# Kernel optimization log

Measured on AMD Instinct MI355X. Metric: run time of the kernel, lower is better.

## Reference

```python
import jax, jax.numpy as jnp
import numpy as np
from jax import lax

EPS = 1e-10

def _ln(x, g, b):
    m = x.mean(-1, keepdims=True)
    v = x.var(-1, keepdims=True)
    return (x - m) / jnp.sqrt(v + 1e-5) * g + b

def _gather(t, idx):
    # t: (B, HW, c), idx: (B, HW, d) -> (B, HW, d, c); out[n,i,k,:] = t[n, idx[n,i,k], :]
    return jax.vmap(lambda tn, In: tn[In])(t, idx)

def setup_inputs() -> dict:
    key = jax.random.key(0)
    ks = jax.random.split(key, 20)
    b, v, c, d, h, w, hid, ksz = 2, 2, 128, 64, 64, 64, 256, 5
    hw = h * w
    Bf = b * v  # v_1 == 1 target view per reference view
    std = 0.02
    return {
        'features_mv': jax.random.normal(ks[0], (b, v, c, h, w), jnp.float32),
        'warp_indices': jax.random.randint(ks[1], (Bf, hw, d), 0, hw, jnp.int32),
        'depth_prob': jax.random.uniform(ks[2], (Bf, hw, d), jnp.float32),
        'ln1_g': jnp.ones((c,), jnp.float32), 'ln1_b': jnp.zeros((c,), jnp.float32),
        'wq': jax.random.normal(ks[3], (c, c), jnp.float32) * std, 'bq': jnp.zeros((c,), jnp.float32),
        'wk': jax.random.normal(ks[4], (c, c), jnp.float32) * std, 'bk': jnp.zeros((c,), jnp.float32),
        'wv': jax.random.normal(ks[5], (c, c), jnp.float32) * std, 'bv': jnp.zeros((c,), jnp.float32),
        'k_pe': jax.random.normal(ks[6], (1, 1, d), jnp.float32) * std,
        'v_pe': jax.random.normal(ks[7], (1, 1, d), jnp.float32) * std,
        'rpe': jax.random.normal(ks[8], (1, 1, d), jnp.float32) * std,
        'proj_w': jax.random.normal(ks[9], (c, c), jnp.float32) * std, 'proj_b': jnp.zeros((c,), jnp.float32),
        'ln2_g': jnp.ones((c,), jnp.float32), 'ln2_b': jnp.zeros((c,), jnp.float32),
        'fc1_w': jax.random.normal(ks[10], (c, hid), jnp.float32) * std, 'fc1_b': jnp.zeros((hid,), jnp.float32),
        'dw_w': jax.random.normal(ks[11], (hid, 1, ksz, ksz), jnp.float32) * std, 'dw_b': jnp.zeros((hid,), jnp.float32),
        'fc2_w': jax.random.normal(ks[12], (hid, c), jnp.float32) * std, 'fc2_b': jnp.zeros((c,), jnp.float32),
    }

def reference(features_mv, warp_indices, depth_prob, ln1_g, ln1_b, wq, bq, wk, bk, wv, bv,
              k_pe, v_pe, rpe, proj_w, proj_b, ln2_g, ln2_b, fc1_w, fc1_b, dw_w, dw_b, fc2_w, fc2_b):
    b, v, c, h, w = features_mv.shape
    hw = h * w
    hid = fc1_w.shape[1]
    scale = c ** (-0.5)  # num_heads = 1 -> head_dim = dim

    # (b v) (h w) c
    x = features_mv.reshape(b * v, c, hw).transpose(0, 2, 1)
    shortcut = x
    xn = _ln(x, ln1_g, ln1_b)
    q = xn @ wq + bq
    k = xn @ wk + bk
    vv = xn @ wv + bv

    # nn pairing: v=2, v_1=1 -> each reference view attends the other view
    Q = (q.reshape(b, v, hw, c) * scale).reshape(b * v, hw, c)
    K = k.reshape(b, v, hw, c)[:, ::-1].reshape(b * v, hw, c)
    V = vv.reshape(b, v, hw, c)[:, ::-1].reshape(b * v, hw, c)

    # SMM_QmK: cost[n,i,k] = sum_c Q[n,i,c] * K[n, idx[n,i,k], c]
    Kg = _gather(K, warp_indices)                       # (B, hw, d, c)
    cost = jnp.einsum('bic,bikc->bik', Q, Kg)
    Q_pe = Q.sum(-1, keepdims=True)                     # (B, hw, 1)
    cost = cost + Q_pe * k_pe + rpe                     # broadcast (1,1,d)

    # (Sim_UNet similarity refinement omitted: UNetModel source unavailable; identity here)
    attn = jax.nn.softmax(cost, axis=-1)
    attn = attn * depth_prob
    attn = (attn + EPS) / (attn.sum(-1, keepdims=True) + EPS)

    # SMM_AmV: out[n,i,c] = sum_k attn[n,i,k] * V[n, idx[n,i,k], c]
    Vg = _gather(V, warp_indices)                       # (B, hw, d, c)
    out = jnp.einsum('bik,bikc->bic', attn, Vg)
    out = out + (attn * v_pe).sum(-1, keepdims=True)

    # projection + residual (v_1 == 1 so B == b*v)
    x = shortcut + (out @ proj_w + proj_b)

    # ConvFFN residual branch
    xn2 = _ln(x, ln2_g, ln2_b)
    y = jax.nn.gelu(xn2 @ fc1_w + fc1_b, approximate=False)
    yi = y.transpose(0, 2, 1).reshape(b * v, hid, h, w)
    yc = lax.conv_general_dilated(yi, dw_w, (1, 1), 'SAME', feature_group_count=hid,
                                  dimension_numbers=('NCHW', 'OIHW', 'NCHW'))
    yc = jax.nn.gelu(yc + dw_b[None, :, None, None], approximate=False)
    y = y + yc.reshape(b * v, hid, hw).transpose(0, 2, 1)
    y = y @ fc2_w + fc2_b
    return x + y
```

## Files before the change

kernel.cpp:

```cpp
#include <hip/hip_runtime.h>
#include <math.h>

#define TOK   16384
#define HW    4096
#define C     128
#define D     64
#define HID   256

constexpr float LN_EPS = 1e-5f;
constexpr float EPS_R  = 1e-10f;
constexpr float QSCALE = 0.08838834764831845f;

typedef __attribute__((ext_vector_type(8))) short  bf16x8;
typedef __attribute__((ext_vector_type(4))) float  f32x4;
typedef __attribute__((ext_vector_type(2))) _Float16 half2v;
#define MFMA16(a, b, c) __builtin_amdgcn_mfma_f32_16x16x32_bf16((a), (b), (c), 0, 0, 0)

__device__ __forceinline__ float bflo(unsigned u) { return __uint_as_float(u << 16); }
__device__ __forceinline__ float bfhi(unsigned u) { return __uint_as_float(u & 0xffff0000u); }
__device__ __forceinline__ float bfu(unsigned short u) { return __uint_as_float((unsigned)u << 16); }
__device__ __forceinline__ unsigned short f2bf(float f) {
  unsigned u = __float_as_uint(f);
  unsigned r = (u + 0x7fffu + ((u >> 16) & 1u)) >> 16;
  return (unsigned short)r;
}
__device__ __forceinline__ unsigned short f2h(float f) {
  _Float16 h = (_Float16)f;
  unsigned short r;
  __builtin_memcpy(&r, &h, 2);
  return r;
}
__device__ __forceinline__ float gelu_exact(float x) {
  return 0.5f * x * (1.0f + erff(x * 0.7071067811865476f));
}

union U4H { uint4 v; half2v h[4]; };
union U1H { unsigned v; half2v h; };

#if __has_builtin(__builtin_amdgcn_fdot2)
__device__ __forceinline__ float dot2h(half2v a, half2v b, float c) {
  return __builtin_amdgcn_fdot2(a, b, c, false);
}
#else
__device__ __forceinline__ float dot2h(half2v a, half2v b, float c) {
  return c + (float)a.x * (float)b.x + (float)a.y * (float)b.y;
}
#endif

__global__ __launch_bounds__(256) void k_prepln1(const float* __restrict__ wq,
    const float* __restrict__ wk, const float* __restrict__ wv,
    const float* __restrict__ pw, const float* __restrict__ f1w,
    const float* __restrict__ f2w, unsigned short* __restrict__ wt,
    const float* __restrict__ feat, const float* __restrict__ g,
    const float* __restrict__ b, unsigned short* __restrict__ xnb) {
  __shared__ float tile[64][C + 1];
  int bidx = blockIdx.x;
  if (bidx < 512) {
    int id = bidx * 256 + threadIdx.x;
    if (id < 16384) {
      int n = id >> 7, k = id & 127;
      wt[id] = f2bf(wq[k * 128 + n]);
    } else if (id < 32768) {
      int e = id - 16384; int n = e >> 7, k = e & 127;
      wt[id] = f2bf(wk[k * 128 + n]);
    } else if (id < 49152) {
      int e = id - 32768; int n = e >> 7, k = e & 127;
      wt[id] = f2bf(wv[k * 128 + n]);
    } else if (id < 65536) {
      int e = id - 49152; int n = e >> 7, k = e & 127;
      wt[id] = f2bf(pw[k * 128 + n]);
    } else if (id < 98304) {
      int e = id - 65536; int n = e >> 7, k = e & 127;
      wt[id] = f2bf(f1w[k * 256 + n]);
    } else {
      int e = id - 98304; int n = e >> 8, k = e & 255;
      wt[id] = f2bf(f2w[k * 128 + n]);
    }
    return;
  }
  int t0 = (bidx - 512) * 64;
  int n = t0 / HW, i0 = t0 % HW;
  int tid = threadIdx.x;
  const float* fb = feat + (size_t)n * C * HW;
  for (int e = tid; e < 64 * C; e += 256) {
    int ch = e >> 6, ii = e & 63;
    tile[ii][ch] = fb[(size_t)ch * HW + i0 + ii];
  }
  __syncthreads();
  int wave = tid >> 6, lane = tid & 63;
  for (int tkn = wave; tkn < 64; tkn += 4) {
    float a0 = tile[tkn][lane];
    float a1 = tile[tkn][lane + 64];
    float s = a0 + a1;
    for (int off = 32; off; off >>= 1) s += __shfl_xor(s, off, 64);
    float mean = s * (1.0f / 128.0f);
    float d0 = a0 - mean, d1 = a1 - mean;
    float v = d0 * d0 + d1 * d1;
    for (int off = 32; off; off >>= 1) v += __shfl_xor(v, off, 64);
    float rstd = rsqrtf(v * (1.0f / 128.0f) + LN_EPS);
    size_t ro = (size_t)(t0 + tkn) * C;
    xnb[ro + lane]      = f2bf(d0 * rstd * g[lane] + b[lane]);
    xnb[ro + lane + 64] = f2bf(d1 * rstd * g[lane + 64] + b[lane + 64]);
  }
}

__global__ __launch_bounds__(256) void k_qkv(const unsigned short* __restrict__ xnb,
    const unsigned short* __restrict__ wt,
    const float* __restrict__ bq, const float* __restrict__ bk,
    const float* __restrict__ bv, unsigned short* __restrict__ qh,
    unsigned short* __restrict__ ksw, unsigned short* __restrict__ vsw) {
  int w = threadIdx.x >> 6, lane = threadIdx.x & 63;
  int q4 = lane >> 4, m = lane & 15;
  int t0 = blockIdx.x * 64 + w * 16;
  int wsel = blockIdx.y;
  const unsigned short* Wt = wt + wsel * 16384;
  const unsigned short* ap = xnb + (size_t)(t0 + m) * C + q4 * 8;
  bf16x8 a[4];
  #pragma unroll
  for (int ks = 0; ks < 4; ks++) a[ks] = *(const bf16x8*)(ap + ks * 32);
  f32x4 acc[8];
  #pragma unroll
  for (int nt = 0; nt < 8; nt++) acc[nt] = (f32x4){0.f, 0.f, 0.f, 0.f};
  #pragma unroll
  for (int nt = 0; nt < 8; nt++) {
    const unsigned short* bp = Wt + (size_t)(nt * 16 + m) * C + q4 * 8;
    #pragma unroll
    for (int ks = 0; ks < 4; ks++) {
      bf16x8 bfrag = *(const bf16x8*)(bp + ks * 32);
      acc[nt] = MFMA16(a[ks], bfrag, acc[nt]);
    }
  }
  const float* B = (wsel == 0) ? bq : ((wsel == 1) ? bk : bv);
  float sc = (wsel == 0) ? QSCALE : 1.0f;
  unsigned short* O = (wsel == 0) ? qh : ((wsel == 1) ? ksw : vsw);
  int n = t0 >> 12, i0 = t0 & 4095;
  int base = (wsel == 0) ? t0 : (((n ^ 1) << 12) + i0);
  #pragma unroll
  for (int nt = 0; nt < 8; nt++) {
    int col = nt * 16 + m;
    float bb = B[col];
    #pragma unroll
    for (int reg = 0; reg < 4; reg++) {
      int row = base + q4 * 4 + reg;
      O[(size_t)row * C + col] = f2h((acc[nt][reg] + bb) * sc);
    }
  }
}

__global__ __launch_bounds__(256) void k_attn(const unsigned short* __restrict__ qh,
    const unsigned short* __restrict__ ksw, const unsigned short* __restrict__ vsw,
    const int* __restrict__ widx, const float* __restrict__ dprob,
    const float* __restrict__ kpe, const float* __restrict__ vpe,
    const float* __restrict__ rpe, unsigned short* __restrict__ aoutb) {
  int lane = threadIdx.x & 63;
  int wave = threadIdx.x >> 6;
  int bid = blockIdx.x;
  int n = (bid >> 1) & 3;
  int within = ((bid >> 3) << 1) | (bid & 1);
  int token = n * HW + within * 4 + wave;
  const unsigned short* Kb = ksw + (size_t)n * HW * C;
  const unsigned short* Vb = vsw + (size_t)n * HW * C;
  int g = lane >> 3, s = lane & 7;
  int myidx = widx[token * D + lane];
  float mydp = dprob[token * D + lane];
  half2v qreg[8];
  {
    const unsigned short* qp = qh + (size_t)token * C + s * 16;
    U4H qa, qb2;
    qa.v = *(const uint4*)(qp);
    qb2.v = *(const uint4*)(qp + 8);
    #pragma unroll
    for (int i = 0; i < 4; i++) { qreg[i] = qa.h[i]; qreg[4 + i] = qb2.h[i]; }
  }
  half2v ones = {(_Float16)1.0f, (_Float16)1.0f};
  float qpe = 0.f;
  #pragma unroll
  for (int i = 0; i < 8; i++) qpe = dot2h(qreg[i], ones, qpe);
  qpe += __shfl_xor(qpe, 1, 64);
  qpe += __shfl_xor(qpe, 2, 64);
  qpe += __shfl_xor(qpe, 4, 64);
  int rowv[8];
  #pragma unroll
  for (int pass = 0; pass < 8; ++pass)
    rowv[pass] = __shfl(myidx, pass * 8 + g, 64);
  uint4 ka[8], kb[8];
  #pragma unroll
  for (int pass = 0; pass < 8; ++pass) {
    const unsigned short* kr = Kb + (size_t)rowv[pass] * C + s * 16;
    ka[pass] = *(const uint4*)(kr);
    kb[pass] = *(const uint4*)(kr + 8);
  }
  float mycost = 0.f;
  #pragma unroll
  for (int pass = 0; pass < 8; ++pass) {
    U4H ua, ub;
    ua.v = ka[pass]; ub.v = kb[pass];
    float p = 0.f;
    #pragma unroll
    for (int i = 0; i < 4; i++) p = dot2h(ua.h[i], qreg[i], p);
    #pragma unroll
    for (int i = 0; i < 4; i++) p = dot2h(ub.h[i], qreg[4 + i], p);
    p += __shfl_xor(p, 1, 64);
    p += __shfl_xor(p, 2, 64);
    p += __shfl_xor(p, 4, 64);
    float t = __shfl(p, (lane & 7) << 3, 64);
    if (pass == g) mycost = t;
  }
  mycost += qpe * kpe[lane] + rpe[lane];
  float mx = mycost;
  for (int off = 32; off; off >>= 1) mx = fmaxf(mx, __shfl_xor(mx, off, 64));
  float e = __expf(mycost - mx);
  float ssum = e;
  for (int off = 32; off; off >>= 1) ssum += __shfl_xor(ssum, off, 64);
  float attn = (e / ssum) * mydp;
  float s2 = attn;
  for (int off = 32; off; off >>= 1) s2 += __shfl_xor(s2, off, 64);
  attn = (attn + EPS_R) / (s2 + EPS_R);
  float vpt = attn * vpe[lane];
  for (int off = 32; off; off >>= 1) vpt += __shfl_xor(vpt, off, 64);
  float o0 = vpt, o1 = vpt;
  unsigned att_u = __float_as_uint(attn);
  #pragma unroll
  for (int blk = 0; blk < 8; ++blk) {
    unsigned vv[8];
    #pragma unroll
    for (int j = 0; j < 8; j++) {
      int row = __builtin_amdgcn_readlane(myidx, blk * 8 + j);
      vv[j] = *(const unsigned*)(Vb + (size_t)row * C + lane * 2);
    }
    #pragma unroll
    for (int j = 0; j < 8; j++) {
      float a = __uint_as_float(__builtin_amdgcn_readlane(att_u, blk * 8 + j));
      U1H h; h.v = vv[j];
      o0 += a * (float)h.h.x;
      o1 += a * (float)h.h.y;
    }
  }
  unsigned pk = (unsigned)f2bf(o0) | ((unsigned)f2bf(o1) << 16);
  *(unsigned*)(aoutb + (size_t)token * C + lane * 2) = pk;
}

__global__ __launch_bounds__(256) void k_projln(const unsigned short* __restrict__ aoutb,
    const unsigned short* __restrict__ wt, const float* __restrict__ pb,
    const float* __restrict__ feat, float* __restrict__ xio,
    const float* __restrict__ g2, const float* __restrict__ b2,
    unsigned short* __restrict__ xn2b) {
  int w = threadIdx.x >> 6, lane = threadIdx.x & 63;
  int q4 = lane >> 4, m = lane & 15;
  int t0 = blockIdx.x * 64 + w * 16;
  const unsigned short* Wt = wt + 3 * 16384;
  const unsigned short* ap = aoutb + (size_t)(t0 + m) * C + q4 * 8;
  bf16x8 a[4];
  #pragma unroll
  for (int ks = 0; ks < 4; ks++) a[ks] = *(const bf16x8*)(ap + ks * 32);
  f32x4 acc[8];
  #pragma unroll
  for (int nt = 0; nt < 8; nt++) acc[nt] = (f32x4){0.f, 0.f, 0.f, 0.f};
  #pragma unroll
  for (int nt = 0; nt < 8; nt++) {
    const unsigned short* bp = Wt + (size_t)(nt * 16 + m) * C + q4 * 8;
    #pragma unroll
    for (int ks = 0; ks < 4; ks++) {
      bf16x8 bfrag = *(const bf16x8*)(bp + ks * 32);
      acc[nt] = MFMA16(a[ks], bfrag, acc[nt]);
    }
  }
  int nview = t0 >> 12, ibase = (t0 & 4095) + q4 * 4;
  float s1[4] = {0.f, 0.f, 0.f, 0.f}, s2[4] = {0.f, 0.f, 0.f, 0.f};
  #pragma unroll
  for (int nt = 0; nt < 8; nt++) {
    int col = nt * 16 + m;
    float bb = pb[col];
    const float* fp = feat + ((size_t)nview * C + col) * HW + ibase;
    #pragma unroll
    for (int reg = 0; reg < 4; reg++) {
      float v = acc[nt][reg] + bb + fp[reg];
      acc[nt][reg] = v;
      s1[reg] += v;
      s2[reg] += v * v;
    }
  }
  #pragma unroll
  for (int reg = 0; reg < 4; reg++) {
    #pragma unroll
    for (int off = 1; off < 16; off <<= 1) {
      s1[reg] += __shfl_xor(s1[reg], off, 64);
      s2[reg] += __shfl_xor(s2[reg], off, 64);
    }
  }
  float mean[4], rstd[4];
  #pragma unroll
  for (int reg = 0; reg < 4; reg++) {
    mean[reg] = s1[reg] * (1.0f / 128.0f);
    float var = s2[reg] * (1.0f / 128.0f) - mean[reg] * mean[reg];
    rstd[reg] = rsqrtf(var + LN_EPS);
  }
  #pragma unroll
  for (int nt = 0; nt < 8; nt++) {
    int col = nt * 16 + m;
    float gc = g2[col], bc = b2[col];
    #pragma unroll
    for (int reg = 0; reg < 4; reg++) {
      int row = t0 + q4 * 4 + reg;
      float v = acc[nt][reg];
      xio[(size_t)row * C + col] = v;
      xn2b[(size_t)row * C + col] = f2bf((v - mean[reg]) * rstd[reg] * gc + bc);
    }
  }
}

__global__ __launch_bounds__(256) void k_fc1(const unsigned short* __restrict__ xn2b,
    const unsigned short* __restrict__ wt, const float* __restrict__ f1b,
    unsigned short* __restrict__ y) {
  int w = threadIdx.x >> 6, lane = threadIdx.x & 63;
  int q4 = lane >> 4, m = lane & 15;
  int t0 = blockIdx.x * 64 + w * 16;
  int n0 = blockIdx.y * 128;
  const unsigned short* Wt = wt + 65536 + (size_t)n0 * C;
  const unsigned short* ap = xn2b + (size_t)(t0 + m) * C + q4 * 8;
  bf16x8 a[4];
  #pragma unroll
  for (int ks = 0; ks < 4; ks++) a[ks] = *(const bf16x8*)(ap + ks * 32);
  f32x4 acc[8];
  #pragma unroll
  for (int nt = 0; nt < 8; nt++) acc[nt] = (f32x4){0.f, 0.f, 0.f, 0.f};
  #pragma unroll
  for (int nt = 0; nt < 8; nt++) {
    const unsigned short* bp = Wt + (size_t)(nt * 16 + m) * C + q4 * 8;
    #pragma unroll
    for (int ks = 0; ks < 4; ks++) {
      bf16x8 bfrag = *(const bf16x8*)(bp + ks * 32);
      acc[nt] = MFMA16(a[ks], bfrag, acc[nt]);
    }
  }
  #pragma unroll
  for (int nt = 0; nt < 8; nt++) {
    int col = n0 + nt * 16 + m;
    float bb = f1b[col];
    #pragma unroll
    for (int reg = 0; reg < 4; reg++) {
      int row = t0 + q4 * 4 + reg;
      y[(size_t)row * HID + col] = f2bf(gelu_exact(acc[nt][reg] + bb));
    }
  }
}

__global__ __launch_bounds__(256) void k_dwconv(const unsigned short* __restrict__ y,
    const float* __restrict__ w, const float* __restrict__ bias,
    unsigned short* __restrict__ ysum) {
  __shared__ float tile[8][401];
  __shared__ float wl[8][25];
  __shared__ float bl[8];
  int bid = blockIdx.x;
  int tile_id = bid & 15;
  int cb = (bid >> 4) & 31;
  int n = bid >> 9;
  int ty = (tile_id >> 2) * 16, tx = (tile_id & 3) * 16;
  int ch0 = cb * 8;
  int tid = threadIdx.x;
  if (tid < 200) wl[tid / 25][tid % 25] = w[(size_t)(ch0 + tid / 25) * 25 + tid % 25];
  if (tid < 8) bl[tid] = bias[ch0 + tid];
  const unsigned short* yb = y + (size_t)n * HW * HID;
  for (int p = tid; p < 400; p += 256) {
    int py = p / 20, px = p % 20;
    int gy = ty + py - 2, gx = tx + px - 2;
    uint4 v = make_uint4(0u, 0u, 0u, 0u);
    if (gy >= 0 && gy < 64 && gx >= 0 && gx < 64)
      v = *(const uint4*)(yb + (size_t)(gy * 64 + gx) * HID + ch0);
    tile[0][p] = bflo(v.x); tile[1][p] = bfhi(v.x);
    tile[2][p] = bflo(v.y); tile[3][p] = bfhi(v.y);
    tile[4][p] = bflo(v.z); tile[5][p] = bfhi(v.z);
    tile[6][p] = bflo(v.w); tile[7][p] = bfhi(v.w);
  }
  __syncthreads();
  int cc = tid & 7;
  int xx = (tid >> 3) & 15;
  int yg = tid >> 7;
  float wreg[25];
  #pragma unroll
  for (int k = 0; k < 25; k++) wreg[k] = wl[cc][k];
  float bb = bl[cc];
  float win[12][5];
  #pragma unroll
  for (int r = 0; r < 12; r++)
    #pragma unroll
    for (int dx = 0; dx < 5; dx++)
      win[r][dx] = tile[cc][(yg * 8 + r) * 20 + xx + dx];
  #pragma unroll
  for (int j = 0; j < 8; ++j) {
    float acc = 0.f;
    #pragma unroll
    for (int dy = 0; dy < 5; ++dy)
      #pragma unroll
      for (int dx = 0; dx < 5; ++dx)
        acc += wreg[dy * 5 + dx] * win[j + dy][dx];
    float o = win[j + 2][2] + gelu_exact(acc + bb);
    int yy = yg * 8 + j;
    ysum[(size_t)(n * HW + (ty + yy) * 64 + tx + xx) * HID + ch0 + cc] = f2bf(o);
  }
}

__global__ __launch_bounds__(256) void k_fc2(const unsigned short* __restrict__ ysum,
    const unsigned short* __restrict__ wt, const float* __restrict__ f2b,
    const float* __restrict__ xio, float* __restrict__ outp) {
  int w = threadIdx.x >> 6, lane = threadIdx.x & 63;
  int q4 = lane >> 4, m = lane & 15;
  int t0 = blockIdx.x * 64 + w * 16;
  int half = blockIdx.y;
  const unsigned short* Wt = wt + 98304;
  const unsigned short* ap = ysum + (size_t)(t0 + m) * HID + q4 * 8;
  bf16x8 a[8];
  #pragma unroll
  for (int ks = 0; ks < 8; ks++) a[ks] = *(const bf16x8*)(ap + ks * 32);
  f32x4 acc[4];
  #pragma unroll
  for (int nt = 0; nt < 4; nt++) acc[nt] = (f32x4){0.f, 0.f, 0.f, 0.f};
  #pragma unroll
  for (int nt = 0; nt < 4; nt++) {
    const unsigned short* bp = Wt + (size_t)(half * 64 + nt * 16 + m) * HID + q4 * 8;
    #pragma unroll
    for (int ks = 0; ks < 8; ks++) {
      bf16x8 bfrag = *(const bf16x8*)(bp + ks * 32);
      acc[nt] = MFMA16(a[ks], bfrag, acc[nt]);
    }
  }
  #pragma unroll
  for (int nt = 0; nt < 4; nt++) {
    int col = half * 64 + nt * 16 + m;
    float bb = f2b[col];
    #pragma unroll
    for (int reg = 0; reg < 4; reg++) {
      int row = t0 + q4 * 4 + reg;
      outp[(size_t)row * C + col] = acc[nt][reg] + bb + xio[(size_t)row * C + col];
    }
  }
}

extern "C" void kernel_launch(void* const* d_in, const int* in_sizes, int n_in,
                              void* d_out, int out_size, void* d_ws, size_t ws_size,
                              hipStream_t stream) {
  (void)in_sizes; (void)n_in; (void)out_size; (void)ws_size;
  const float* feat  = (const float*)d_in[0];
  const int*   widx  = (const int*)d_in[1];
  const float* dprob = (const float*)d_in[2];
  const float* ln1g  = (const float*)d_in[3];
  const float* ln1b  = (const float*)d_in[4];
  const float* wq    = (const float*)d_in[5];
  const float* bq    = (const float*)d_in[6];
  const float* wk    = (const float*)d_in[7];
  const float* bk    = (const float*)d_in[8];
  const float* wv    = (const float*)d_in[9];
  const float* bv    = (const float*)d_in[10];
  const float* kpe   = (const float*)d_in[11];
  const float* vpe   = (const float*)d_in[12];
  const float* rpe   = (const float*)d_in[13];
  const float* pw    = (const float*)d_in[14];
  const float* pb    = (const float*)d_in[15];
  const float* ln2g  = (const float*)d_in[16];
  const float* ln2b  = (const float*)d_in[17];
  const float* f1w   = (const float*)d_in[18];
  const float* f1b   = (const float*)d_in[19];
  const float* dww   = (const float*)d_in[20];
  const float* dwb   = (const float*)d_in[21];
  const float* f2w   = (const float*)d_in[22];
  const float* f2b   = (const float*)d_in[23];

  float* ws = (float*)d_ws;
  const size_t M2 = (size_t)TOK * C;
  float* xio = ws;
  unsigned short* qhb   = (unsigned short*)(ws + M2);
  unsigned short* xnb   = (unsigned short*)(ws + M2 + M2 / 2);
  unsigned short* ksb   = (unsigned short*)(ws + 2 * M2);
  unsigned short* vsb   = (unsigned short*)(ws + 2 * M2 + M2 / 2);
  unsigned short* aoutb = (unsigned short*)(ws + 3 * M2);
  unsigned short* xn2b  = (unsigned short*)(ws + 3 * M2 + M2 / 2);
  unsigned short* yb    = (unsigned short*)(ws + 4 * M2);
  unsigned short* ysumb = (unsigned short*)(ws + 5 * M2);
  unsigned short* wtb   = (unsigned short*)(ws + 6 * M2);

  k_prepln1<<<512 + TOK / 64, 256, 0, stream>>>(wq, wk, wv, pw, f1w, f2w, wtb,
                                                feat, ln1g, ln1b, xnb);
  k_qkv   <<<dim3(TOK / 64, 3), 256, 0, stream>>>(xnb, wtb, bq, bk, bv, qhb, ksb, vsb);
  k_attn  <<<TOK / 4, 256, 0, stream>>>(qhb, ksb, vsb, widx, dprob, kpe, vpe, rpe, aoutb);
  k_projln<<<TOK / 64, 256, 0, stream>>>(aoutb, wtb, pb, feat, xio, ln2g, ln2b, xn2b);
  k_fc1   <<<dim3(TOK / 64, 2), 256, 0, stream>>>(xn2b, wtb, f1b, yb);
  k_dwconv<<<2048, 256, 0, stream>>>(yb, dww, dwb, ysumb);
  k_fc2   <<<dim3(TOK / 64, 2), 256, 0, stream>>>(ysumb, wtb, f2b, xio, (float*)d_out);
}
```

Baseline: 205.5 us.

## Fuse attention, output projection with LayerNorm, and fc1 into one kernel

Merges the attention gather kernel, the projection+residual+LN2 kernel, and the fc1+GELU kernel into a single kernel. Each 256-thread block handles 16 tokens (4 per wave, looped) and keeps the attention output and the normalized activations in a swizzled shared-memory tile. The 128 projection columns and 256 fc1 columns are split across the 4 waves, and the LayerNorm row sums are combined through shared memory. This removes two launches and the global round trips of aout and xn2. In exchange each wave runs attention serially over 4 tokens, the blocks carry extra barriers, and the grid holds 4x fewer blocks, which may reduce latency hiding for the gather loads.

```diff
diff --git a/kernel.cpp b/kernel.cpp
--- a/kernel.cpp
+++ b/kernel.cpp
@@ -147,131 +147,142 @@
   }
 }
 
-__global__ __launch_bounds__(256) void k_attn(const unsigned short* __restrict__ qh,
-    const unsigned short* __restrict__ ksw, const unsigned short* __restrict__ vsw,
-    const int* __restrict__ widx, const float* __restrict__ dprob,
-    const float* __restrict__ kpe, const float* __restrict__ vpe,
-    const float* __restrict__ rpe, unsigned short* __restrict__ aoutb) {
+__global__ __launch_bounds__(256) void k_attn_proj_fc1(
+    const unsigned short* __restrict__ qh, const unsigned short* __restrict__ ksw,
+    const unsigned short* __restrict__ vsw, const int* __restrict__ widx,
+    const float* __restrict__ dprob, const float* __restrict__ kpe,
+    const float* __restrict__ vpe, const float* __restrict__ rpe,
+    const unsigned short* __restrict__ wt, const float* __restrict__ pb,
+    const float* __restrict__ feat, float* __restrict__ xio,
+    const float* __restrict__ g2, const float* __restrict__ b2,
+    const float* __restrict__ f1b, unsigned short* __restrict__ y) {
+  __shared__ unsigned short axn[16 * C];
+  __shared__ float ps1[4][16];
+  __shared__ float ps2[4][16];
   int lane = threadIdx.x & 63;
   int wave = threadIdx.x >> 6;
   int bid = blockIdx.x;
   int n = (bid >> 1) & 3;
   int within = ((bid >> 3) << 1) | (bid & 1);
-  int token = n * HW + within * 4 + wave;
+  int T0 = n * HW + within * 16;
   const unsigned short* Kb = ksw + (size_t)n * HW * C;
   const unsigned short* Vb = vsw + (size_t)n * HW * C;
-  int g = lane >> 3, s = lane & 7;
-  int myidx = widx[token * D + lane];
-  float mydp = dprob[token * D + lane];
-  half2v qreg[8];
-  {
-    const unsigned short* qp = qh + (size_t)token * C + s * 16;
-    U4H qa, qb2;
-    qa.v = *(const uint4*)(qp);
-    qb2.v = *(const uint4*)(qp + 8);
-    #pragma unroll
-    for (int i = 0; i < 4; i++) { qreg[i] = qa.h[i]; qreg[4 + i] = qb2.h[i]; }
-  }
+  int gg = lane >> 3, s = lane & 7;
   half2v ones = {(_Float16)1.0f, (_Float16)1.0f};
-  float qpe = 0.f;
-  #pragma unroll
-  for (int i = 0; i < 8; i++) qpe = dot2h(qreg[i], ones, qpe);
-  qpe += __shfl_xor(qpe, 1, 64);
-  qpe += __shfl_xor(qpe, 2, 64);
-  qpe += __shfl_xor(qpe, 4, 64);
-  int rowv[8];
-  #pragma unroll
-  for (int pass = 0; pass < 8; ++pass)
-    rowv[pass] = __shfl(myidx, pass * 8 + g, 64);
-  uint4 ka[8], kb[8];
-  #pragma unroll
-  for (int pass = 0; pass < 8; ++pass) {
-    const unsigned short* kr = Kb + (size_t)rowv[pass] * C + s * 16;
-    ka[pass] = *(const uint4*)(kr);
-    kb[pass] = *(const uint4*)(kr + 8);
-  }
-  float mycost = 0.f;
-  #pragma unroll
-  for (int pass = 0; pass < 8; ++pass) {
-    U4H ua, ub;
-    ua.v = ka[pass]; ub.v = kb[pass];
-    float p = 0.f;
-    #pragma unroll
-    for (int i = 0; i < 4; i++) p = dot2h(ua.h[i], qreg[i], p);
-    #pragma unroll
-    for (int i = 0; i < 4; i++) p = dot2h(ub.h[i], qreg[4 + i], p);
-    p += __shfl_xor(p, 1, 64);
-    p += __shfl_xor(p, 2, 64);
-    p += __shfl_xor(p, 4, 64);
-    float t = __shfl(p, (lane & 7) << 3, 64);
-    if (pass == g) mycost = t;
-  }
-  mycost += qpe * kpe[lane] + rpe[lane];
-  float mx = mycost;
-  for (int off = 32; off; off >>= 1) mx = fmaxf(mx, __shfl_xor(mx, off, 64));
-  float e = __expf(mycost - mx);
-  float ssum = e;
-  for (int off = 32; off; off >>= 1) ssum += __shfl_xor(ssum, off, 64);
-  float attn = (e / ssum) * mydp;
-  float s2 = attn;
-  for (int off = 32; off; off >>= 1) s2 += __shfl_xor(s2, off, 64);
-  attn = (attn + EPS_R) / (s2 + EPS_R);
-  float vpt = attn * vpe[lane];
-  for (int off = 32; off; off >>= 1) vpt += __shfl_xor(vpt, off, 64);
-  float o0 = vpt, o1 = vpt;
-  unsigned att_u = __float_as_uint(attn);
-  #pragma unroll
-  for (int blk = 0; blk < 8; ++blk) {
-    unsigned vv[8];
-    #pragma unroll
-    for (int j = 0; j < 8; j++) {
-      int row = __builtin_amdgcn_readlane(myidx, blk * 8 + j);
-      vv[j] = *(const unsigned*)(Vb + (size_t)row * C + lane * 2);
-    }
-    #pragma unroll
-    for (int j = 0; j < 8; j++) {
-      float a = __uint_as_float(__builtin_amdgcn_readlane(att_u, blk * 8 + j));
-      U1H h; h.v = vv[j];
-      o0 += a * (float)h.h.x;
-      o1 += a * (float)h.h.y;
-    }
-  }
-  unsigned pk = (unsigned)f2bf(o0) | ((unsigned)f2bf(o1) << 16);
-  *(unsigned*)(aoutb + (size_t)token * C + lane * 2) = pk;
-}
-
-__global__ __launch_bounds__(256) void k_projln(const unsigned short* __restrict__ aoutb,
-    const unsigned short* __restrict__ wt, const float* __restrict__ pb,
-    const float* __restrict__ feat, float* __restrict__ xio,
-    const float* __restrict__ g2, const float* __restrict__ b2,
-    unsigned short* __restrict__ xn2b) {
-  int w = threadIdx.x >> 6, lane = threadIdx.x & 63;
+
+  for (int tj = 0; tj < 4; ++tj) {
+    int token = T0 + wave * 4 + tj;
+    int myidx = widx[(size_t)token * D + lane];
+    float mydp = dprob[(size_t)token * D + lane];
+    half2v qreg[8];
+    {
+      const unsigned short* qp = qh + (size_t)token * C + s * 16;
+      U4H qa, qb2;
+      qa.v = *(const uint4*)(qp);
+      qb2.v = *(const uint4*)(qp + 8);
+      #pragma unroll
+      for (int i = 0; i < 4; i++) { qreg[i] = qa.h[i]; qreg[4 + i] = qb2.h[i]; }
+    }
+    float qpe = 0.f;
+    #pragma unroll
+    for (int i = 0; i < 8; i++) qpe = dot2h(qreg[i], ones, qpe);
+    qpe += __shfl_xor(qpe, 1, 64);
+    qpe += __shfl_xor(qpe, 2, 64);
+    qpe += __shfl_xor(qpe, 4, 64);
+    int rowv[8];
+    #pragma unroll
+    for (int pass = 0; pass < 8; ++pass)
+      rowv[pass] = __shfl(myidx, pass * 8 + gg, 64);
+    uint4 ka[8], kb[8];
+    #pragma unroll
+    for (int pass = 0; pass < 8; ++pass) {
+      const unsigned short* kr = Kb + (size_t)rowv[pass] * C + s * 16;
+      ka[pass] = *(const uint4*)(kr);
+      kb[pass] = *(const uint4*)(kr + 8);
+    }
+    float mycost = 0.f;
+    #pragma unroll
+    for (int pass = 0; pass < 8; ++pass) {
+      U4H ua, ub;
+      ua.v = ka[pass]; ub.v = kb[pass];
+      float p = 0.f;
+      #pragma unroll
+      for (int i = 0; i < 4; i++) p = dot2h(ua.h[i], qreg[i], p);
+      #pragma unroll
+      for (int i = 0; i < 4; i++) p = dot2h(ub.h[i], qreg[4 + i], p);
+      p += __shfl_xor(p, 1, 64);
+      p += __shfl_xor(p, 2, 64);
+      p += __shfl_xor(p, 4, 64);
+      float t = __shfl(p, (lane & 7) << 3, 64);
+      if (pass == gg) mycost = t;
+    }
+    mycost += qpe * kpe[lane] + rpe[lane];
+    float mx = mycost;
+    for (int off = 32; off; off >>= 1) mx = fmaxf(mx, __shfl_xor(mx, off, 64));
+    float e = __expf(mycost - mx);
+    float ssum = e;
+    for (int off = 32; off; off >>= 1) ssum += __shfl_xor(ssum, off, 64);
+    float attn = (e / ssum) * mydp;
+    float sren = attn;
+    for (int off = 32; off; off >>= 1) sren += __shfl_xor(sren, off, 64);
+    attn = (attn + EPS_R) / (sren + EPS_R);
+    float vpt = attn * vpe[lane];
+    for (int off = 32; off; off >>= 1) vpt += __shfl_xor(vpt, off, 64);
+    float o0 = vpt, o1 = vpt;
+    unsigned att_u = __float_as_uint(attn);
+    #pragma unroll
+    for (int blk = 0; blk < 8; ++blk) {
+      unsigned vv[8];
+      #pragma unroll
+      for (int j = 0; j < 8; j++) {
+        int row = __builtin_amdgcn_readlane(myidx, blk * 8 + j);
+        vv[j] = *(const unsigned*)(Vb + (size_t)row * C + lane * 2);
+      }
+      #pragma unroll
+      for (int j = 0; j < 8; j++) {
+        float a = __uint_as_float(__builtin_amdgcn_readlane(att_u, blk * 8 + j));
+        U1H h; h.v = vv[j];
+        o0 += a * (float)h.h.x;
+        o1 += a * (float)h.h.y;
+      }
+    }
+    unsigned pk = (unsigned)f2bf(o0) | ((unsigned)f2bf(o1) << 16);
+    int row = wave * 4 + tj;
+    int boff = row * 256 + lane * 4;
+    boff ^= (row & 15) << 4;
+    *(unsigned*)((char*)axn + boff) = pk;
+  }
+  __syncthreads();
+
   int q4 = lane >> 4, m = lane & 15;
-  int t0 = blockIdx.x * 64 + w * 16;
-  const unsigned short* Wt = wt + 3 * 16384;
-  const unsigned short* ap = aoutb + (size_t)(t0 + m) * C + q4 * 8;
   bf16x8 a[4];
   #pragma unroll
-  for (int ks = 0; ks < 4; ks++) a[ks] = *(const bf16x8*)(ap + ks * 32);
-  f32x4 acc[8];
-  #pragma unroll
-  for (int nt = 0; nt < 8; nt++) acc[nt] = (f32x4){0.f, 0.f, 0.f, 0.f};
-  #pragma unroll
-  for (int nt = 0; nt < 8; nt++) {
-    const unsigned short* bp = Wt + (size_t)(nt * 16 + m) * C + q4 * 8;
+  for (int ks = 0; ks < 4; ks++) {
+    int boff = m * 256 + ks * 64 + q4 * 16;
+    boff ^= m << 4;
+    a[ks] = *(const bf16x8*)((char*)axn + boff);
+  }
+  const unsigned short* Wp = wt + 3 * 16384;
+  f32x4 acc[2];
+  #pragma unroll
+  for (int nt = 0; nt < 2; nt++) acc[nt] = (f32x4){0.f, 0.f, 0.f, 0.f};
+  #pragma unroll
+  for (int nt = 0; nt < 2; nt++) {
+    int colt = wave * 32 + nt * 16;
+    const unsigned short* bp = Wp + (size_t)(colt + m) * C + q4 * 8;
     #pragma unroll
     for (int ks = 0; ks < 4; ks++) {
       bf16x8 bfrag = *(const bf16x8*)(bp + ks * 32);
       acc[nt] = MFMA16(a[ks], bfrag, acc[nt]);
     }
   }
-  int nview = t0 >> 12, ibase = (t0 & 4095) + q4 * 4;
+  int ibase = (T0 & 4095) + q4 * 4;
   float s1[4] = {0.f, 0.f, 0.f, 0.f}, s2[4] = {0.f, 0.f, 0.f, 0.f};
   #pragma unroll
-  for (int nt = 0; nt < 8; nt++) {
-    int col = nt * 16 + m;
+  for (int nt = 0; nt < 2; nt++) {
+    int col = wave * 32 + nt * 16 + m;
     float bb = pb[col];
-    const float* fp = feat + ((size_t)nview * C + col) * HW + ibase;
+    const float* fp = feat + ((size_t)n * C + col) * HW + ibase;
     #pragma unroll
     for (int reg = 0; reg < 4; reg++) {
       float v = acc[nt][reg] + bb + fp[reg];
@@ -288,59 +299,70 @@
       s2[reg] += __shfl_xor(s2[reg], off, 64);
     }
   }
+  if (m == 0) {
+    #pragma unroll
+    for (int reg = 0; reg < 4; reg++) {
+      ps1[wave][q4 * 4 + reg] = s1[reg];
+      ps2[wave][q4 * 4 + reg] = s2[reg];
+    }
+  }
+  __syncthreads();
   float mean[4], rstd[4];
   #pragma unroll
   for (int reg = 0; reg < 4; reg++) {
-    mean[reg] = s1[reg] * (1.0f / 128.0f);
-    float var = s2[reg] * (1.0f / 128.0f) - mean[reg] * mean[reg];
+    int row = q4 * 4 + reg;
+    float t1 = ps1[0][row] + ps1[1][row] + ps1[2][row] + ps1[3][row];
+    float t2 = ps2[0][row] + ps2[1][row] + ps2[2][row] + ps2[3][row];
+    mean[reg] = t1 * (1.0f / 128.0f);
+    float var = t2 * (1.0f / 128.0f) - mean[reg] * mean[reg];
     rstd[reg] = rsqrtf(var + LN_EPS);
   }
   #pragma unroll
-  for (int nt = 0; nt < 8; nt++) {
-    int col = nt * 16 + m;
+  for (int nt = 0; nt < 2; nt++) {
+    int col = wave * 32 + nt * 16 + m;
     float gc = g2[col], bc = b2[col];
     #pragma unroll
     for (int reg = 0; reg < 4; reg++) {
-      int row = t0 + q4 * 4 + reg;
+      int row = q4 * 4 + reg;
       float v = acc[nt][reg];
-      xio[(size_t)row * C + col] = v;
-      xn2b[(size_t)row * C + col] = f2bf((v - mean[reg]) * rstd[reg] * gc + bc);
-    }
-  }
-}
-
-__global__ __launch_bounds__(256) void k_fc1(const unsigned short* __restrict__ xn2b,
-    const unsigned short* __restrict__ wt, const float* __restrict__ f1b,
-    unsigned short* __restrict__ y) {
-  int w = threadIdx.x >> 6, lane = threadIdx.x & 63;
-  int q4 = lane >> 4, m = lane & 15;
-  int t0 = blockIdx.x * 64 + w * 16;
-  int n0 = blockIdx.y * 128;
-  const unsigned short* Wt = wt + 65536 + (size_t)n0 * C;
-  const unsigned short* ap = xn2b + (size_t)(t0 + m) * C + q4 * 8;
-  bf16x8 a[4];
-  #pragma unroll
-  for (int ks = 0; ks < 4; ks++) a[ks] = *(const bf16x8*)(ap + ks * 32);
-  f32x4 acc[8];
-  #pragma unroll
-  for (int nt = 0; nt < 8; nt++) acc[nt] = (f32x4){0.f, 0.f, 0.f, 0.f};
-  #pragma unroll
-  for (int nt = 0; nt < 8; nt++) {
-    const unsigned short* bp = Wt + (size_t)(nt * 16 + m) * C + q4 * 8;
+      xio[(size_t)(T0 + row) * C + col] = v;
+      unsigned short xv = f2bf((v - mean[reg]) * rstd[reg] * gc + bc);
+      int boff = row * 256 + col * 2;
+      boff ^= (row & 15) << 4;
+      *(unsigned short*)((char*)axn + boff) = xv;
+    }
+  }
+  __syncthreads();
+
+  bf16x8 af[4];
+  #pragma unroll
+  for (int ks = 0; ks < 4; ks++) {
+    int boff = m * 256 + ks * 64 + q4 * 16;
+    boff ^= m << 4;
+    af[ks] = *(const bf16x8*)((char*)axn + boff);
+  }
+  const unsigned short* Wf = wt + 65536;
+  f32x4 acc2[4];
+  #pragma unroll
+  for (int nt = 0; nt < 4; nt++) acc2[nt] = (f32x4){0.f, 0.f, 0.f, 0.f};
+  #pragma unroll
+  for (int nt = 0; nt < 4; nt++) {
+    int colt = wave * 64 + nt * 16;
+    const unsigned short* bp = Wf + (size_t)(colt + m) * C + q4 * 8;
     #pragma unroll
     for (int ks = 0; ks < 4; ks++) {
       bf16x8 bfrag = *(const bf16x8*)(bp + ks * 32);
-      acc[nt] = MFMA16(a[ks], bfrag, acc[nt]);
-    }
-  }
-  #pragma unroll
-  for (int nt = 0; nt < 8; nt++) {
-    int col = n0 + nt * 16 + m;
+      acc2[nt] = MFMA16(af[ks], bfrag, acc2[nt]);
+    }
+  }
+  #pragma unroll
+  for (int nt = 0; nt < 4; nt++) {
+    int col = wave * 64 + nt * 16 + m;
     float bb = f1b[col];
     #pragma unroll
     for (int reg = 0; reg < 4; reg++) {
-      int row = t0 + q4 * 4 + reg;
-      y[(size_t)row * HID + col] = f2bf(gelu_exact(acc[nt][reg] + bb));
+      int row = T0 + q4 * 4 + reg;
+      y[(size_t)row * HID + col] = f2bf(gelu_exact(acc2[nt][reg] + bb));
     }
   }
 }
@@ -472,18 +494,16 @@
   unsigned short* xnb   = (unsigned short*)(ws + M2 + M2 / 2);
   unsigned short* ksb   = (unsigned short*)(ws + 2 * M2);
   unsigned short* vsb   = (unsigned short*)(ws + 2 * M2 + M2 / 2);
-  unsigned short* aoutb = (unsigned short*)(ws + 3 * M2);
-  unsigned short* xn2b  = (unsigned short*)(ws + 3 * M2 + M2 / 2);
-  unsigned short* yb    = (unsigned short*)(ws + 4 * M2);
-  unsigned short* ysumb = (unsigned short*)(ws + 5 * M2);
-  unsigned short* wtb   = (unsigned short*)(ws + 6 * M2);
+  unsigned short* yb    = (unsigned short*)(ws + 3 * M2);
+  unsigned short* ysumb = (unsigned short*)(ws + 4 * M2);
+  unsigned short* wtb   = (unsigned short*)(ws + 5 * M2);
 
   k_prepln1<<<512 + TOK / 64, 256, 0, stream>>>(wq, wk, wv, pw, f1w, f2w, wtb,
                                                 feat, ln1g, ln1b, xnb);
   k_qkv   <<<dim3(TOK / 64, 3), 256, 0, stream>>>(xnb, wtb, bq, bk, bv, qhb, ksb, vsb);
-  k_attn  <<<TOK / 4, 256, 0, stream>>>(qhb, ksb, vsb, widx, dprob, kpe, vpe, rpe, aoutb);
-  k_projln<<<TOK / 64, 256, 0, stream>>>(aoutb, wtb, pb, feat, xio, ln2g, ln2b, xn2b);
-  k_fc1   <<<dim3(TOK / 64, 2), 256, 0, stream>>>(xn2b, wtb, f1b, yb);
+  k_attn_proj_fc1<<<TOK / 16, 256, 0, stream>>>(qhb, ksb, vsb, widx, dprob, kpe, vpe,
+                                                rpe, wtb, pb, feat, xio, ln2g, ln2b,
+                                                f1b, yb);
   k_dwconv<<<2048, 256, 0, stream>>>(yb, dww, dwb, ysumb);
   k_fc2   <<<dim3(TOK / 64, 2), 256, 0, stream>>>(ysumb, wtb, f2b, xio, (float*)d_out);
 }
```

Result: slower. 209.8 us (+2.1%).
